# Kernel tuning notes

Hardware: AMD Instinct MI355X
Metric: run time of the kernel (lower is better)

Reference implementation:

```python
import jax, jax.numpy as jnp
from jax import lax
import numpy as np

B = 16384


def setup_inputs() -> dict:
    key = jax.random.key(0)
    ks = jax.random.split(key, 8)
    g = lambda k, s: jax.random.normal(k, s, jnp.float32) * 0.05
    return {
        'data': (jax.random.uniform(ks[0], (B, 10, 10, 1)) > 0.9).astype(jnp.float32),
        'w1': g(ks[1], (3, 3, 1, 128)),   'b1': jnp.zeros((128,), jnp.float32),
        'w2': g(ks[2], (3, 3, 128, 128)), 'b2': jnp.zeros((128,), jnp.float32),
        'w3': g(ks[3], (3, 3, 128, 64)),  'b3': jnp.zeros((64,), jnp.float32),
        'w4': g(ks[4], (3, 3, 64, 64)),   'b4': jnp.zeros((64,), jnp.float32),
        'wd1': g(ks[5], (64, 32)), 'bd1': jnp.zeros((32,), jnp.float32),
        'wd2': g(ks[6], (32, 4)),  'bd2': jnp.zeros((4,), jnp.float32),
    }


DN = ('NHWC', 'HWIO', 'NHWC')


def _conv(x, w, b):
    return jax.nn.relu(lax.conv_general_dilated(x, w, (1, 1), 'SAME', dimension_numbers=DN) + b)


def _pool(x):  # MaxPooling2D(pool=2, strides=2, valid)
    return lax.reduce_window(x, -jnp.inf, lax.max, (1, 2, 2, 1), (1, 2, 2, 1), 'VALID')


def reference(data, w1, b1, w2, b2, w3, b3, w4, b4, wd1, bd1, wd2, bd2):
    H = W = 10.0
    x = _pool(_conv(_conv(data, w1, b1), w2, b2))          # [B,5,5,128]
    x = _pool(_conv(_conv(x, w3, b3), w4, b4))             # [B,2,2,64]
    x = jnp.mean(x, axis=(1, 2))                           # GAP -> [B,64]
    x = jax.nn.relu(x @ wd1 + bd1)
    svg = jax.nn.sigmoid(x @ wd2 + bd2).reshape(-1, 2, 2)  # [B,2,2]
    p1 = svg[:, 0, :, None]                                # [B,2,1]
    p2 = svg[:, 1, :, None]
    t = jnp.linspace(0.0, 1.0, 5)
    pts = ((1.0 - t) * p1 + t * p2).transpose(0, 2, 1)     # [B,5,2]
    pts = pts * jnp.array([H, W], jnp.float32)
    # straight-through round
    pts = pts + lax.stop_gradient(jnp.round(pts) - pts)
    # sort by linearized position
    pos = pts[:, :, 0] * W + pts[:, :, 1]
    order = jnp.argsort(pos, axis=1)
    pts = jnp.take_along_axis(pts, order[:, :, None], axis=1)
    # dedup: keep point i if L1 distance to previous point != 0 (first always kept)
    d = jnp.sum(jnp.abs(pts[:, 1:] - pts[:, :-1]), axis=2)           # [B,4]
    d = jnp.concatenate([jnp.ones((d.shape[0], 1), d.dtype), d], 1)  # [B,5]
    keep = d != 0.0
    dest = jnp.where(keep, jnp.cumsum(keep.astype(jnp.int32), axis=1) - 1, 5)
    out = jnp.full((pts.shape[0], 6, 2), -1.0, pts.dtype)  # slot 5 = trash
    out = out.at[jnp.arange(pts.shape[0])[:, None], dest].set(pts)
    return out[:, :5]                                      # [B,5,2], padded with -1
```

## Files before the change

### kernel.cpp

```cpp
#include <hip/hip_runtime.h>
#include <hip/hip_bf16.h>
#include <math.h>

typedef float f4 __attribute__((ext_vector_type(4)));
typedef float f32x4 __attribute__((ext_vector_type(4)));
typedef __bf16 bf16x8 __attribute__((ext_vector_type(8)));
typedef unsigned int uint32x4 __attribute__((ext_vector_type(4)));

#define NT 256

__global__ void repack_w(const float* __restrict__ w1, const float* __restrict__ w2,
                         const float* __restrict__ w3, const float* __restrict__ w4,
                         __hip_bfloat16* __restrict__ ws)
{
    int tid = blockIdx.x * 256 + threadIdx.x;
    const int T2 = 147456, T3 = 73728, T4 = 36864, T1 = 4096;
    if (tid < T2) {
        int j = tid & 7, l = (tid >> 3) & 63, rest = tid >> 9;
        int n = rest & 7, kidx = rest >> 3;
        int cs = kidx & 3, tap = kidx >> 2;
        int ci = cs * 32 + ((l >> 4) << 3) + j;
        int co = (n << 4) + (l & 15);
        ws[tid] = __float2bfloat16(w2[(tap * 128 + ci) * 128 + co]);
    } else if (tid < T2 + T3) {
        int t3 = tid - T2;
        int j = t3 & 7, l = (t3 >> 3) & 63, rest = t3 >> 9;
        int n = rest & 3, kidx = rest >> 2;
        int cs = kidx & 3, tap = kidx >> 2;
        int ci = cs * 32 + ((l >> 4) << 3) + j;
        int co = (n << 4) + (l & 15);
        ws[tid] = __float2bfloat16(w3[(tap * 128 + ci) * 64 + co]);
    } else if (tid < T2 + T3 + T4) {
        int t4 = tid - T2 - T3;
        int j = t4 & 7, l = (t4 >> 3) & 63, rest = t4 >> 9;
        int n = rest & 3, ks = rest >> 2;
        int half = ks & 1, tap = ks >> 1;
        int ci = half * 32 + ((l >> 4) << 3) + j;
        int co = (n << 4) + (l & 15);
        ws[tid] = __float2bfloat16(w4[(tap * 64 + ci) * 64 + co]);
    } else if (tid < T2 + T3 + T4 + T1) {
        int t1 = tid - T2 - T3 - T4;
        int j = t1 & 7, l = (t1 >> 3) & 63, n = (t1 >> 9) & 7;
        int k = ((l >> 4) << 3) + j;
        int co = (n << 4) + (l & 15);
        float v = (k < 9) ? w1[k * 128 + co] : 0.f;
        ws[tid] = __float2bfloat16(v);
    }
}

__global__ __launch_bounds__(NT, 4)
void img2svg_fused(const float* __restrict__ data,
                   const float* __restrict__ b1, const float* __restrict__ b2,
                   const float* __restrict__ b3, const float* __restrict__ b4,
                   const float* __restrict__ wd1, const float* __restrict__ bd1,
                   const float* __restrict__ wd2, const float* __restrict__ bd2,
                   const __hip_bfloat16* __restrict__ wsb,
                   float* __restrict__ out)
{
    __shared__ __align__(16) unsigned char s_u[33280];
    __shared__ float s_in[144];
    __shared__ float s_pool4[4 * 64];
    __shared__ float s_feat[64];
    __shared__ float s_h[32];

    const int t = threadIdx.x;
    const int img = blockIdx.x;
    const int w = t >> 6;
    const int lane = t & 63;
    const int kg = lane >> 4;
    const int l15 = lane & 15;
    const int kgbase1 = kg * 1616;
    const int kgbase2 = kg * 416;

    if (t < 144) {
        int r = t / 12, c = t % 12;
        float v = 0.f;
        if (r >= 1 && r <= 10 && c >= 1 && c <= 10)
            v = data[img * 100 + (r - 1) * 10 + (c - 1)];
        s_in[t] = v;
    }
    if (t < 128)
        *(__bf16*)(s_u + (t >> 3) * 1616 + 1600 + (t & 7) * 2) = (__bf16)0.f;
    s_pool4[t] = 0.f;
    __syncthreads();

    {
        const uint32x4* pk1v = (const uint32x4*)((const __hip_bfloat16*)wsb + 258048);
        uint32x4 B0 = pk1v[((w * 2 + 0) << 6) + lane];
        uint32x4 B1 = pk1v[((w * 2 + 1) << 6) + lane];
        float bj0 = b1[(w * 2 + 0) * 16 + l15];
        float bj1 = b1[(w * 2 + 1) * 16 + l15];
        const int kb0 = (w * 2 + 0) * 2 + (l15 >> 3);
        const int kb1 = (w * 2 + 1) * 2 + (l15 >> 3);
        const int cb = (l15 & 7) * 2;

        for (int mi = 0; mi < 7; ++mi) {
            int p_raw = mi * 16 + l15;
            int p = p_raw < 100 ? p_raw : 99;
            int y = p / 10, x = p - 10 * (p / 10);
            bf16x8 A = __builtin_bit_cast(bf16x8, (uint32x4){0, 0, 0, 0});
            if (kg == 0) {
#pragma unroll
                for (int j = 0; j < 8; ++j)
                    A[j] = (__bf16)s_in[(y + j / 3) * 12 + x + j % 3];
            } else if (kg == 1) {
                A[0] = (__bf16)s_in[(y + 2) * 12 + x + 2];
            }
            f32x4 c0 = (f32x4){bj0, bj0, bj0, bj0};
            f32x4 c1 = (f32x4){bj1, bj1, bj1, bj1};
            c0 = __builtin_amdgcn_mfma_f32_16x16x32_bf16(
                A, __builtin_bit_cast(bf16x8, B0), c0, 0, 0, 0);
            c1 = __builtin_amdgcn_mfma_f32_16x16x32_bf16(
                A, __builtin_bit_cast(bf16x8, B1), c1, 0, 0, 0);
#pragma unroll
            for (int rr = 0; rr < 4; ++rr) {
                int p_out = mi * 16 + kg * 4 + rr;
                if (p_out < 100) {
                    *(__bf16*)(s_u + kb0 * 1616 + p_out * 16 + cb) =
                        (__bf16)fmaxf(c0[rr], 0.f);
                    *(__bf16*)(s_u + kb1 * 1616 + p_out * 16 + cb) =
                        (__bf16)fmaxf(c1[rr], 0.f);
                }
            }
        }
    }
    __syncthreads();

    {
        const uint32x4* pk2v = (const uint32x4*)wsb;

        f32x4 acc[7][2];
#pragma unroll
        for (int j = 0; j < 2; ++j) {
            float bj = b2[(w * 2 + j) * 16 + l15];
#pragma unroll
            for (int mi = 0; mi < 7; ++mi) acc[mi][j] = (f32x4){bj, bj, bj, bj};
        }

        int pos[7];
#pragma unroll
        for (int mi = 0; mi < 7; ++mi) pos[mi] = mi * 16 + l15;

        for (int tap = 0; tap < 9; ++tap) {
            const int dy = tap / 3, dx = tap - 3 * (tap / 3);
            int ao[7];
#pragma unroll
            for (int mi = 0; mi < 7; ++mi) {
                int py = pos[mi] / 10;
                int px = pos[mi] - 10 * py;
                int ay = py + dy - 1, ax = px + dx - 1;
                int r = ((unsigned)ay < 10u && (unsigned)ax < 10u) ? ay * 10 + ax : 100;
                ao[mi] = (r << 4) + kgbase1;
            }
#pragma unroll
            for (int cs = 0; cs < 4; ++cs) {
                int ks = tap * 4 + cs;
                uint32x4 Bc0 = pk2v[(((ks << 3) + w * 2 + 0) << 6) + lane];
                uint32x4 Bc1 = pk2v[(((ks << 3) + w * 2 + 1) << 6) + lane];
#pragma unroll
                for (int mi = 0; mi < 7; ++mi) {
                    bf16x8 A = *(const bf16x8*)(const void*)(s_u + cs * 6464 + ao[mi]);
                    acc[mi][0] = __builtin_amdgcn_mfma_f32_16x16x32_bf16(
                        A, __builtin_bit_cast(bf16x8, Bc0), acc[mi][0], 0, 0, 0);
                    acc[mi][1] = __builtin_amdgcn_mfma_f32_16x16x32_bf16(
                        A, __builtin_bit_cast(bf16x8, Bc1), acc[mi][1], 0, 0, 0);
                }
                __builtin_amdgcn_sched_group_barrier(0x020, 2, 0);
#pragma unroll
                for (int g = 0; g < 7; ++g) {
                    __builtin_amdgcn_sched_group_barrier(0x100, 1, 0);
                    __builtin_amdgcn_sched_group_barrier(0x008, 2, 0);
                }
            }
        }
        __syncthreads();

        float* xp = (float*)s_u;
#pragma unroll
        for (int mi = 0; mi < 7; ++mi) {
            int posb = mi * 16 + kg * 4;
            if (mi < 6 || kg == 0) {
                int s = posb >> 1;
#pragma unroll
                for (int j = 0; j < 2; ++j) {
                    int co = (w * 2 + j) * 16 + l15;
                    float m01 = fmaxf(fmaxf(acc[mi][j][0], acc[mi][j][1]), 0.f);
                    float m23 = fmaxf(fmaxf(acc[mi][j][2], acc[mi][j][3]), 0.f);
                    xp[s * 132 + co] = m01;
                    xp[(s + 1) * 132 + co] = m23;
                }
            }
        }
    }
    __syncthreads();

    {
        const float* xp = (const float*)s_u;
        for (int i = t; i < 3200; i += NT) {
            int r = i >> 7, c = i & 127;
            int y2 = r / 5, x2 = r - 5 * y2;
            int s = y2 * 10 + x2;
            float v = fmaxf(xp[s * 132 + c], xp[(s + 5) * 132 + c]);
            *(__bf16*)(s_u + 26400 + (c >> 3) * 416 + (r << 4) + (c & 7) * 2) = (__bf16)v;
        }
        if (t < 128)
            *(__bf16*)(s_u + 26400 + (t >> 3) * 416 + 400 + (t & 7) * 2) = (__bf16)0.f;
    }
    __syncthreads();

    {
        if (t < 64)
            *(__bf16*)(s_u + (t >> 3) * 416 + 400 + (t & 7) * 2) = (__bf16)0.f;

        const int mt = w & 1, ntp = w >> 1;
        const uint32x4* pk3v = (const uint32x4*)((const __hip_bfloat16*)wsb + 147456);

        f32x4 c3[2];
#pragma unroll
        for (int j = 0; j < 2; ++j) {
            float bj = b3[ntp * 32 + j * 16 + l15];
            c3[j] = (f32x4){bj, bj, bj, bj};
        }
        int pos = mt * 16 + l15;
        int p3y = pos / 5, p3x = pos - 5 * (pos / 5);

        uint32x4 Bc[2], Bn[2];
#pragma unroll
        for (int j = 0; j < 2; ++j) Bc[j] = pk3v[((ntp * 2 + j) << 6) + lane];

        for (int tap = 0; tap < 9; ++tap) {
            const int dy = tap / 3, dx = tap - 3 * (tap / 3);
            int ay = p3y + dy - 1, ax = p3x + dx - 1;
            int r = ((unsigned)ay < 5u && (unsigned)ax < 5u) ? ay * 5 + ax : 25;
            int ao = 26400 + (r << 4) + kgbase2;
#pragma unroll
            for (int cs = 0; cs < 4; ++cs) {
                int nk = tap * 4 + cs + 1;
                if (nk < 36) {
#pragma unroll
                    for (int j = 0; j < 2; ++j)
                        Bn[j] = pk3v[(((nk << 2) + ntp * 2 + j) << 6) + lane];
                }
                bf16x8 A = *(const bf16x8*)(const void*)(s_u + cs * 1664 + ao);
#pragma unroll
                for (int j = 0; j < 2; ++j)
                    c3[j] = __builtin_amdgcn_mfma_f32_16x16x32_bf16(
                        A, __builtin_bit_cast(bf16x8, Bc[j]), c3[j], 0, 0, 0);
#pragma unroll
                for (int j = 0; j < 2; ++j) Bc[j] = Bn[j];
            }
        }
#pragma unroll
        for (int j = 0; j < 2; ++j) {
            int co = ntp * 32 + j * 16 + l15;
            int kb = co >> 3, cb = (co & 7) * 2;
#pragma unroll
            for (int rr = 0; rr < 4; ++rr) {
                int p = mt * 16 + kg * 4 + rr;
                if (p < 25)
                    *(__bf16*)(s_u + kb * 416 + p * 16 + cb) =
                        (__bf16)fmaxf(c3[j][rr], 0.f);
            }
        }
    }
    __syncthreads();

    {
        const int nt = w;
        const uint32x4* pk4v = (const uint32x4*)((const __hip_bfloat16*)wsb + 221184);
        float bj = b4[nt * 16 + l15];
        f32x4 c4 = (f32x4){bj, bj, bj, bj};
        int py = l15 >> 2, px = l15 & 3;

        uint32x4 Bc = pk4v[(nt << 6) + lane], Bn;
        for (int ks = 0; ks < 18; ++ks) {
            if (ks < 17) Bn = pk4v[((((ks + 1) << 2) + nt) << 6) + lane];
            int half = ks & 1, tap = ks >> 1;
            int dy = tap / 3, dx = tap - 3 * (tap / 3);
            int ay = py + dy - 1, ax = px + dx - 1;
            int r = ((unsigned)ay < 5u && (unsigned)ax < 5u) ? ay * 5 + ax : 25;
            bf16x8 A = *(const bf16x8*)(const void*)(
                s_u + (half * 4 + kg) * 416 + (r << 4));
            c4 = __builtin_amdgcn_mfma_f32_16x16x32_bf16(
                A, __builtin_bit_cast(bf16x8, Bc), c4, 0, 0, 0);
            Bc = Bn;
        }
#pragma unroll
        for (int rr = 0; rr < 4; ++rr) {
            int p = kg * 4 + rr;
            int cell = ((p >> 2) >> 1) * 2 + ((p & 3) >> 1);
            float rv = fmaxf(c4[rr], 0.f);
            atomicMax((int*)&s_pool4[cell * 64 + nt * 16 + l15], __float_as_int(rv));
        }
    }
    __syncthreads();

    if (t < 64) {
        float f = 0.25f * (s_pool4[t] + s_pool4[64 + t] + s_pool4[128 + t] + s_pool4[192 + t]);
        s_feat[t] = f;
    }
    __syncthreads();
    if (t < 32) {
        float h = bd1[t];
        for (int i = 0; i < 64; ++i) h = fmaf(s_feat[i], wd1[i * 32 + t], h);
        s_h[t] = fmaxf(h, 0.f);
    }
    __syncthreads();

    if (t == 0) {
        float v[4];
#pragma unroll
        for (int o = 0; o < 4; ++o) {
            float vv = bd2[o];
            for (int i = 0; i < 32; ++i) vv = fmaf(s_h[i], wd2[i * 4 + o], vv);
            v[o] = 1.f / (1.f + expf(-vv));
        }
        float px[5], py[5], pp[5];
#pragma unroll
        for (int k = 0; k < 5; ++k) {
            float tk = 0.25f * (float)k;
            float gx = ((1.f - tk) * v[0] + tk * v[2]) * 10.f;
            float gy = ((1.f - tk) * v[1] + tk * v[3]) * 10.f;
            px[k] = rintf(gx);
            py[k] = rintf(gy);
            pp[k] = px[k] * 10.f + py[k];
        }
#pragma unroll
        for (int pass = 0; pass < 4; ++pass)
#pragma unroll
            for (int i = 0; i < 4 - pass; ++i) {
                bool sw = pp[i] > pp[i + 1];
                float a, b;
                a = pp[i]; b = pp[i + 1]; pp[i] = sw ? b : a; pp[i + 1] = sw ? a : b;
                a = px[i]; b = px[i + 1]; px[i] = sw ? b : a; px[i + 1] = sw ? a : b;
                a = py[i]; b = py[i + 1]; py[i] = sw ? b : a; py[i + 1] = sw ? a : b;
            }
        float* op = out + img * 10;
#pragma unroll
        for (int i = 0; i < 5; ++i) { op[2 * i] = -1.f; op[2 * i + 1] = -1.f; }
        int k2 = 0;
#pragma unroll
        for (int i = 0; i < 5; ++i) {
            bool keep;
            if (i == 0) keep = true;
            else keep = (fabsf(px[i] - px[i - 1]) + fabsf(py[i] - py[i - 1])) != 0.f;
            if (keep) {
                op[2 * k2] = px[i];
                op[2 * k2 + 1] = py[i];
                ++k2;
            }
        }
    }
}

extern "C" void kernel_launch(void* const* d_in, const int* in_sizes, int n_in,
                              void* d_out, int out_size, void* d_ws, size_t ws_size,
                              hipStream_t stream) {
    const float* data = (const float*)d_in[0];
    const float* w1  = (const float*)d_in[1];
    const float* b1  = (const float*)d_in[2];
    const float* w2  = (const float*)d_in[3];
    const float* b2  = (const float*)d_in[4];
    const float* w3  = (const float*)d_in[5];
    const float* b3  = (const float*)d_in[6];
    const float* w4  = (const float*)d_in[7];
    const float* b4  = (const float*)d_in[8];
    const float* wd1 = (const float*)d_in[9];
    const float* bd1 = (const float*)d_in[10];
    const float* wd2 = (const float*)d_in[11];
    const float* bd2 = (const float*)d_in[12];
    float* out = (float*)d_out;
    __hip_bfloat16* wsb = (__hip_bfloat16*)d_ws;

    repack_w<<<1024, 256, 0, stream>>>(w1, w2, w3, w4, wsb);

    int nimg = in_sizes[0] / 100;
    img2svg_fused<<<nimg, NT, 0, stream>>>(data, b1, b2, b3, b4,
                                           wd1, bd1, wd2, bd2, wsb, out);
}
```

Measured before the change: 635.3 us.

## Switch conv2 to 32x32x16 MFMA with 2x2 wave tiling

Conv2's implicit GEMM moves from 16x16x32 bf16 MFMA tiles (7 M-tiles per wave, each wave owning 32 output channels) to 32x32x16 MFMA on a 2x2 wave grid, where each wave owns 64 positions by 64 channels. The w2 repack is rearranged to match the new B operand layout, and the pooling epilogue is rewritten for the 32x32 accumulator layout. The intent is fewer A-operand LDS reads per MFMA and less redundant padding (128 rows instead of 112, still over 100 positions), at the cost of more accumulator registers and twice as many K-steps, each with its own B loads.

```diff
diff --git a/kernel.cpp b/kernel.cpp
--- a/kernel.cpp
+++ b/kernel.cpp
@@ -4,6 +4,7 @@
 
 typedef float f4 __attribute__((ext_vector_type(4)));
 typedef float f32x4 __attribute__((ext_vector_type(4)));
+typedef float f32x16 __attribute__((ext_vector_type(16)));
 typedef __bf16 bf16x8 __attribute__((ext_vector_type(8)));
 typedef unsigned int uint32x4 __attribute__((ext_vector_type(4)));
 
@@ -17,10 +18,10 @@
     const int T2 = 147456, T3 = 73728, T4 = 36864, T1 = 4096;
     if (tid < T2) {
         int j = tid & 7, l = (tid >> 3) & 63, rest = tid >> 9;
-        int n = rest & 7, kidx = rest >> 3;
-        int cs = kidx & 3, tap = kidx >> 2;
-        int ci = cs * 32 + ((l >> 4) << 3) + j;
-        int co = (n << 4) + (l & 15);
+        int n = rest & 3, kstep = rest >> 2;
+        int k = kstep * 16 + ((l >> 5) << 3) + j;
+        int tap = k >> 7, ci = k & 127;
+        int co = n * 32 + (l & 31);
         ws[tid] = __float2bfloat16(w2[(tap * 128 + ci) * 128 + co]);
     } else if (tid < T2 + T3) {
         int t3 = tid - T2;
@@ -69,7 +70,6 @@
     const int lane = t & 63;
     const int kg = lane >> 4;
     const int l15 = lane & 15;
-    const int kgbase1 = kg * 1616;
     const int kgbase2 = kg * 416;
 
     if (t < 144) {
@@ -128,46 +128,54 @@
 
     {
         const uint32x4* pk2v = (const uint32x4*)wsb;
-
-        f32x4 acc[7][2];
-#pragma unroll
-        for (int j = 0; j < 2; ++j) {
-            float bj = b2[(w * 2 + j) * 16 + l15];
-#pragma unroll
-            for (int mi = 0; mi < 7; ++mi) acc[mi][j] = (f32x4){bj, bj, bj, bj};
-        }
-
-        int pos[7];
-#pragma unroll
-        for (int mi = 0; mi < 7; ++mi) pos[mi] = mi * 16 + l15;
+        const int wm = w >> 1, wn = w & 1;
+        const int l31 = lane & 31;
+        const int l5h = lane >> 5;
+        const int kbb = l5h * 1616;
+
+        f32x16 acc[2][2];
+#pragma unroll
+        for (int nj = 0; nj < 2; ++nj) {
+            float bj = b2[(wn * 2 + nj) * 32 + l31];
+#pragma unroll
+            for (int mi = 0; mi < 2; ++mi)
+#pragma unroll
+                for (int rg = 0; rg < 16; ++rg) acc[mi][nj][rg] = bj;
+        }
+
+        int pyA[2], pxA[2];
+#pragma unroll
+        for (int mi = 0; mi < 2; ++mi) {
+            int pos = (wm * 2 + mi) * 32 + l31;
+            pyA[mi] = pos / 10;
+            pxA[mi] = pos - 10 * pyA[mi];
+        }
 
         for (int tap = 0; tap < 9; ++tap) {
             const int dy = tap / 3, dx = tap - 3 * (tap / 3);
-            int ao[7];
-#pragma unroll
-            for (int mi = 0; mi < 7; ++mi) {
-                int py = pos[mi] / 10;
-                int px = pos[mi] - 10 * py;
-                int ay = py + dy - 1, ax = px + dx - 1;
+            int ao[2];
+#pragma unroll
+            for (int mi = 0; mi < 2; ++mi) {
+                int ay = pyA[mi] + dy - 1, ax = pxA[mi] + dx - 1;
                 int r = ((unsigned)ay < 10u && (unsigned)ax < 10u) ? ay * 10 + ax : 100;
-                ao[mi] = (r << 4) + kgbase1;
-            }
-#pragma unroll
-            for (int cs = 0; cs < 4; ++cs) {
-                int ks = tap * 4 + cs;
-                uint32x4 Bc0 = pk2v[(((ks << 3) + w * 2 + 0) << 6) + lane];
-                uint32x4 Bc1 = pk2v[(((ks << 3) + w * 2 + 1) << 6) + lane];
-#pragma unroll
-                for (int mi = 0; mi < 7; ++mi) {
-                    bf16x8 A = *(const bf16x8*)(const void*)(s_u + cs * 6464 + ao[mi]);
-                    acc[mi][0] = __builtin_amdgcn_mfma_f32_16x16x32_bf16(
-                        A, __builtin_bit_cast(bf16x8, Bc0), acc[mi][0], 0, 0, 0);
-                    acc[mi][1] = __builtin_amdgcn_mfma_f32_16x16x32_bf16(
-                        A, __builtin_bit_cast(bf16x8, Bc1), acc[mi][1], 0, 0, 0);
+                ao[mi] = (r << 4) + kbb;
+            }
+#pragma unroll
+            for (int ksl = 0; ksl < 8; ++ksl) {
+                int kstep = tap * 8 + ksl;
+                uint32x4 B0 = pk2v[((kstep * 4 + wn * 2 + 0) << 6) + lane];
+                uint32x4 B1 = pk2v[((kstep * 4 + wn * 2 + 1) << 6) + lane];
+#pragma unroll
+                for (int mi = 0; mi < 2; ++mi) {
+                    bf16x8 A = *(const bf16x8*)(const void*)(s_u + ksl * 3232 + ao[mi]);
+                    acc[mi][0] = __builtin_amdgcn_mfma_f32_32x32x16_bf16(
+                        A, __builtin_bit_cast(bf16x8, B0), acc[mi][0], 0, 0, 0);
+                    acc[mi][1] = __builtin_amdgcn_mfma_f32_32x32x16_bf16(
+                        A, __builtin_bit_cast(bf16x8, B1), acc[mi][1], 0, 0, 0);
                 }
                 __builtin_amdgcn_sched_group_barrier(0x020, 2, 0);
 #pragma unroll
-                for (int g = 0; g < 7; ++g) {
+                for (int g = 0; g < 2; ++g) {
                     __builtin_amdgcn_sched_group_barrier(0x100, 1, 0);
                     __builtin_amdgcn_sched_group_barrier(0x008, 2, 0);
                 }
@@ -177,20 +185,24 @@
 
         float* xp = (float*)s_u;
 #pragma unroll
-        for (int mi = 0; mi < 7; ++mi) {
-            int posb = mi * 16 + kg * 4;
-            if (mi < 6 || kg == 0) {
-                int s = posb >> 1;
-#pragma unroll
-                for (int j = 0; j < 2; ++j) {
-                    int co = (w * 2 + j) * 16 + l15;
-                    float m01 = fmaxf(fmaxf(acc[mi][j][0], acc[mi][j][1]), 0.f);
-                    float m23 = fmaxf(fmaxf(acc[mi][j][2], acc[mi][j][3]), 0.f);
-                    xp[s * 132 + co] = m01;
-                    xp[(s + 1) * 132 + co] = m23;
-                }
-            }
-        }
+        for (int mi = 0; mi < 2; ++mi)
+#pragma unroll
+            for (int q = 0; q < 4; ++q) {
+                int base = (wm * 2 + mi) * 32 + 8 * q + 4 * l5h;
+                if (base < 100) {
+                    int s = base >> 1;
+#pragma unroll
+                    for (int nj = 0; nj < 2; ++nj) {
+                        int co = (wn * 2 + nj) * 32 + l31;
+                        float m01 = fmaxf(fmaxf(acc[mi][nj][q * 4 + 0],
+                                                acc[mi][nj][q * 4 + 1]), 0.f);
+                        float m23 = fmaxf(fmaxf(acc[mi][nj][q * 4 + 2],
+                                                acc[mi][nj][q * 4 + 3]), 0.f);
+                        xp[s * 132 + co] = m01;
+                        xp[(s + 1) * 132 + co] = m23;
+                    }
+                }
+            }
     }
     __syncthreads();
 
```

Result: slower. 694.1 us (+9.3%).
